# Performance work log

Hardware: AMD Instinct MI355X
Metric: run time of the kernel (lower is better)

Reference implementation:

```python
import jax, jax.numpy as jnp
import numpy as np

HEIGHT, WIDTH = 384, 640


def setup_inputs() -> dict:
    key = jax.random.key(0)
    ks = jax.random.split(key, 6)
    B, N, C_CLS, D = 8, 100, 92, 256
    return {
        "images": jax.random.normal(ks[0], (B, 3, HEIGHT, WIDTH), dtype=jnp.float32),
        "logits": jax.random.normal(ks[1], (B, N, C_CLS), dtype=jnp.float32),
        "pred_boxes": jax.random.uniform(ks[2], (B, N, 4), dtype=jnp.float32),
        "last_hidden_state": jax.random.normal(ks[3], (B, N, D), dtype=jnp.float32),
        "fc_w": jax.random.normal(ks[4], (256, D), dtype=jnp.float32) * 0.05,
        "fc_b": jax.random.normal(ks[5], (256,), dtype=jnp.float32) * 0.05,
    }


def reference(images, logits, pred_boxes, last_hidden_state, fc_w, fc_b):
    B = images.shape[0]
    num_objects = 2

    # probas computed in the original forward (unused in training mode -> DCE'd)
    probas = jax.nn.softmax(logits, axis=-1)[:, :, :-1]

    # cxcywh -> xyxy, scale by [W, H, W, H], truncate to int (torch .int())
    cx, cy, w, h = jnp.split(pred_boxes, 4, axis=-1)  # each [B, N, 1]
    xyxy = jnp.concatenate([cx - 0.5 * w, cy - 0.5 * h, cx + 0.5 * w, cy + 0.5 * h], axis=-1)
    img_dims = jnp.array([WIDTH, HEIGHT, WIDTH, HEIGHT], dtype=jnp.float32)
    bboxes = (xyxy * img_dims).astype(jnp.int32)  # [B, N, 4]

    # bboxes_to_mask (faithful to original, incl. its x/y axis convention):
    # x indexes rows (height), y indexes columns (width)
    x = jnp.arange(HEIGHT, dtype=jnp.float32)[:, None]   # [H, 1]
    y = jnp.arange(WIDTH, dtype=jnp.float32)[None, :]    # [1, W]
    bb = bboxes.astype(jnp.float32)[:, :, :, None, None]  # [B, N, 4, 1, 1]
    masks = (bb[:, :, 0] <= x) & (x <= bb[:, :, 2]) & (bb[:, :, 1] <= y) & (y <= bb[:, :, 3])  # [B, N, H, W]

    # diff images: sum channels, pairwise diff over (pre, post), abs, repeat x2 on batch
    summed = images.sum(axis=1).reshape(B // 2, 2, HEIGHT, WIDTH)
    diff = jnp.abs(summed[:, 1:] - summed[:, :1])          # [B/2, 1, H, W]
    diff = jnp.repeat(diff, 2, axis=0)                     # [B, 1, H, W]

    # masked mean score per box
    scores = jnp.mean(jnp.where(masks, diff, jnp.float32(0.0)), axis=(2, 3))  # [B, N]

    _, indices = jax.lax.top_k(scores, num_objects)        # [B, num_objects]
    h_i = jnp.take_along_axis(last_hidden_state, indices[:, :, None], axis=1)  # [B, O, D]
    h_i = h_i @ fc_w.T + fc_b                              # Linear: x W^T + b
    h_i = h_i.reshape(B // 2, 2, num_objects, -1)          # [b, i=2, O, hidden]
    return h_i[:, 0], h_i[:, 1]
```

## Files before the change

### kernel.cpp

```cpp
#include <hip/hip_runtime.h>

#define H_IMG 384
#define W_IMG 640
#define NPAIR 4
#define NBATCH 8
#define NBOX 100
#define DHID 256
#define ROWTILE 24
#define NTILES (H_IMG / ROWTILE)

__global__ __launch_bounds__(256) void k_diff_rowscan(const float* __restrict__ images,
                                                      float* __restrict__ sat) {
    const int row = blockIdx.x * 4 + (threadIdx.x >> 6);
    const int lane = threadIdx.x & 63;
    const int p = row / H_IMG;
    const int h = row - p * H_IMG;

    const size_t chw = (size_t)H_IMG * W_IMG;
    const float* i0 = images + ((size_t)(2 * p)     * 3 * H_IMG + h) * W_IMG;
    const float* i1 = images + ((size_t)(2 * p + 1) * 3 * H_IMG + h) * W_IMG;
    float* srow = sat + ((size_t)p * H_IMG + h) * W_IMG;

    float carry = 0.0f;
    #pragma unroll
    for (int k = 0; k < W_IMG / 64; ++k) {
        const int w = k * 64 + lane;
        float s0 = (i0[w] + i0[w + chw]) + i0[w + 2 * chw];
        float s1 = (i1[w] + i1[w + chw]) + i1[w + 2 * chw];
        float v = fabsf(s1 - s0);
        #pragma unroll
        for (int off = 1; off < 64; off <<= 1) {
            float u = __shfl_up(v, off, 64);
            if (lane >= off) v += u;
        }
        v += carry;
        srow[w] = v;
        carry = __shfl(v, 63, 64);
    }
}

__global__ __launch_bounds__(64) void k_colscan_local(float* __restrict__ sat,
                                                      float* __restrict__ totals) {
    const int bid = blockIdx.x;
    const int p  = bid / (10 * NTILES);
    const int r1 = bid - p * (10 * NTILES);
    const int t  = r1 / 10;
    const int cg = r1 - t * 10;
    const int c  = cg * 64 + (int)threadIdx.x;

    float* base = sat + ((size_t)p * H_IMG + t * ROWTILE) * W_IMG + c;
    float run = 0.0f;
    #pragma unroll
    for (int i = 0; i < ROWTILE; ++i) {
        run += base[(size_t)i * W_IMG];
        base[(size_t)i * W_IMG] = run;
    }
    totals[((size_t)p * NTILES + t) * W_IMG + c] = run;
}

__global__ __launch_bounds__(256) void k_score_topk_fc(
        const float* __restrict__ sat,
        const float* __restrict__ totals,
        const float* __restrict__ pred_boxes,
        const float* __restrict__ lhs,
        const float* __restrict__ fc_w,
        const float* __restrict__ fc_b,
        float* __restrict__ out) {
    const int b = blockIdx.x;
    const int t = threadIdx.x;
    const int p = b >> 1;

    __shared__ float s_off[NTILES][W_IMG];
    __shared__ float s_score[NBOX];
    __shared__ int   s_idx[2];
    __shared__ float s_h[2][DHID];

    for (int c = t; c < W_IMG; c += 256) {
        float run = 0.0f;
        #pragma unroll
        for (int tt = 0; tt < NTILES; ++tt) {
            s_off[tt][c] = run;
            run += totals[((size_t)p * NTILES + tt) * W_IMG + c];
        }
    }
    __syncthreads();

    const float* S = sat + (size_t)p * H_IMG * W_IMG;

    if (t < NBOX) {
        const float* pb = pred_boxes + ((size_t)b * NBOX + t) * 4;
        const float cx = pb[0], cy = pb[1], bw = pb[2], bh = pb[3];
        const int bb0 = (int)((cx - 0.5f * bw) * 640.0f);
        const int bb1 = (int)((cy - 0.5f * bh) * 384.0f);
        const int bb2 = (int)((cx + 0.5f * bw) * 640.0f);
        const int bb3 = (int)((cy + 0.5f * bh) * 384.0f);
        const int r0 = bb0 > 0 ? bb0 : 0;
        const int r2 = bb2 < H_IMG - 1 ? bb2 : H_IMG - 1;
        const int c0 = bb1 > 0 ? bb1 : 0;
        const int c2 = bb3 < W_IMG - 1 ? bb3 : W_IMG - 1;
        float sc = 0.0f;
        if (r0 <= r2 && c0 <= c2) {
            float sum = S[(size_t)r2 * W_IMG + c2] + s_off[r2 / ROWTILE][c2];
            if (r0 > 0) sum -= S[(size_t)(r0 - 1) * W_IMG + c2] + s_off[(r0 - 1) / ROWTILE][c2];
            if (c0 > 0) sum -= S[(size_t)r2 * W_IMG + (c0 - 1)] + s_off[r2 / ROWTILE][c0 - 1];
            if (r0 > 0 && c0 > 0)
                sum += S[(size_t)(r0 - 1) * W_IMG + (c0 - 1)] + s_off[(r0 - 1) / ROWTILE][c0 - 1];
            sc = sum / (float)(H_IMG * W_IMG);
        }
        s_score[t] = sc;
    }
    __syncthreads();

    if (t == 0) {
        float b0 = -1e30f, b1 = -1e30f;
        int i0 = 0, i1 = 0;
        for (int n = 0; n < NBOX; ++n) {
            const float s = s_score[n];
            if (s > b0)      { b1 = b0; i1 = i0; b0 = s; i0 = n; }
            else if (s > b1) { b1 = s; i1 = n; }
        }
        s_idx[0] = i0;
        s_idx[1] = i1;
    }
    __syncthreads();

    s_h[0][t] = lhs[((size_t)b * NBOX + s_idx[0]) * DHID + t];
    s_h[1][t] = lhs[((size_t)b * NBOX + s_idx[1]) * DHID + t];
    __syncthreads();

    const float* wrow = fc_w + (size_t)t * DHID;
    float acc0 = fc_b[t];
    float acc1 = acc0;
    #pragma unroll 4
    for (int d = 0; d < DHID; ++d) {
        const float wv = wrow[d];
        acc0 = fmaf(s_h[0][d], wv, acc0);
        acc1 = fmaf(s_h[1][d], wv, acc1);
    }

    const size_t base = (size_t)(b & 1) * (NPAIR * 2 * DHID) + (size_t)(b >> 1) * (2 * DHID);
    out[base + t]        = acc0;
    out[base + DHID + t] = acc1;
}

extern "C" void kernel_launch(void* const* d_in, const int* in_sizes, int n_in,
                              void* d_out, int out_size, void* d_ws, size_t ws_size,
                              hipStream_t stream) {
    const float* images     = (const float*)d_in[0];
    const float* pred_boxes = (const float*)d_in[2];
    const float* lhs        = (const float*)d_in[3];
    const float* fc_w       = (const float*)d_in[4];
    const float* fc_b       = (const float*)d_in[5];
    float* out              = (float*)d_out;

    float* sat    = (float*)d_ws;
    float* totals = sat + (size_t)NPAIR * H_IMG * W_IMG;

    hipLaunchKernelGGL(k_diff_rowscan, dim3(NPAIR * H_IMG / 4), dim3(256), 0, stream,
                       images, sat);
    hipLaunchKernelGGL(k_colscan_local, dim3(NPAIR * 10 * NTILES), dim3(64), 0, stream,
                       sat, totals);
    hipLaunchKernelGGL(k_score_topk_fc, dim3(NBATCH), dim3(256), 0, stream,
                       sat, totals, pred_boxes, lhs, fc_w, fc_b, out);
}
```

Baseline: 101.0 us.

## Fuse three kernels into one cooperative kernel with grid syncs

Replaces the three separate launches (diff+row scan, column-tile scan, score/topk/fc) with one cooperative kernel of 256 blocks that loops over the work items and uses grid-wide syncs between the phases. It also vectorises the fc weight loads to float4. The goal is to remove inter-kernel launch gaps. In exchange it adds grid.sync overhead and runs the memory-bound row-scan phase on fewer blocks than before (256 instead of 384), which could reduce achieved bandwidth.

```diff
diff --git a/kernel.cpp b/kernel.cpp
--- a/kernel.cpp
+++ b/kernel.cpp
@@ -1,4 +1,7 @@
 #include <hip/hip_runtime.h>
+#include <hip/hip_cooperative_groups.h>
+
+namespace cg = cooperative_groups;
 
 #define H_IMG 384
 #define W_IMG 640
@@ -8,72 +11,76 @@
 #define DHID 256
 #define ROWTILE 24
 #define NTILES (H_IMG / ROWTILE)
+#define NBLOCKS 256
+#define NWAVES (NBLOCKS * 4)
 
-__global__ __launch_bounds__(256) void k_diff_rowscan(const float* __restrict__ images,
-                                                      float* __restrict__ sat) {
-    const int row = blockIdx.x * 4 + (threadIdx.x >> 6);
-    const int lane = threadIdx.x & 63;
-    const int p = row / H_IMG;
-    const int h = row - p * H_IMG;
-
-    const size_t chw = (size_t)H_IMG * W_IMG;
-    const float* i0 = images + ((size_t)(2 * p)     * 3 * H_IMG + h) * W_IMG;
-    const float* i1 = images + ((size_t)(2 * p + 1) * 3 * H_IMG + h) * W_IMG;
-    float* srow = sat + ((size_t)p * H_IMG + h) * W_IMG;
-
-    float carry = 0.0f;
-    #pragma unroll
-    for (int k = 0; k < W_IMG / 64; ++k) {
-        const int w = k * 64 + lane;
-        float s0 = (i0[w] + i0[w + chw]) + i0[w + 2 * chw];
-        float s1 = (i1[w] + i1[w + chw]) + i1[w + 2 * chw];
-        float v = fabsf(s1 - s0);
-        #pragma unroll
-        for (int off = 1; off < 64; off <<= 1) {
-            float u = __shfl_up(v, off, 64);
-            if (lane >= off) v += u;
-        }
-        v += carry;
-        srow[w] = v;
-        carry = __shfl(v, 63, 64);
-    }
-}
-
-__global__ __launch_bounds__(64) void k_colscan_local(float* __restrict__ sat,
-                                                      float* __restrict__ totals) {
-    const int bid = blockIdx.x;
-    const int p  = bid / (10 * NTILES);
-    const int r1 = bid - p * (10 * NTILES);
-    const int t  = r1 / 10;
-    const int cg = r1 - t * 10;
-    const int c  = cg * 64 + (int)threadIdx.x;
-
-    float* base = sat + ((size_t)p * H_IMG + t * ROWTILE) * W_IMG + c;
-    float run = 0.0f;
-    #pragma unroll
-    for (int i = 0; i < ROWTILE; ++i) {
-        run += base[(size_t)i * W_IMG];
-        base[(size_t)i * W_IMG] = run;
-    }
-    totals[((size_t)p * NTILES + t) * W_IMG + c] = run;
-}
-
-__global__ __launch_bounds__(256) void k_score_topk_fc(
-        const float* __restrict__ sat,
-        const float* __restrict__ totals,
+__global__ __launch_bounds__(256, 1) void k_fused(
+        const float* __restrict__ images,
+        float* __restrict__ sat,
+        float* __restrict__ totals,
         const float* __restrict__ pred_boxes,
         const float* __restrict__ lhs,
         const float* __restrict__ fc_w,
         const float* __restrict__ fc_b,
         float* __restrict__ out) {
-    const int b = blockIdx.x;
+    cg::grid_group grid = cg::this_grid();
     const int t = threadIdx.x;
-    const int p = b >> 1;
+    const int lane = t & 63;
+    const int wid = blockIdx.x * 4 + (t >> 6);
+
+    const size_t chw = (size_t)H_IMG * W_IMG;
+    for (int row = wid; row < NPAIR * H_IMG; row += NWAVES) {
+        const int p = row / H_IMG;
+        const int h = row - p * H_IMG;
+        const float* i0 = images + ((size_t)(2 * p)     * 3 * H_IMG + h) * W_IMG;
+        const float* i1 = images + ((size_t)(2 * p + 1) * 3 * H_IMG + h) * W_IMG;
+        float* srow = sat + ((size_t)p * H_IMG + h) * W_IMG;
+
+        float carry = 0.0f;
+        #pragma unroll
+        for (int k = 0; k < W_IMG / 64; ++k) {
+            const int w = k * 64 + lane;
+            float s0 = (i0[w] + i0[w + chw]) + i0[w + 2 * chw];
+            float s1 = (i1[w] + i1[w + chw]) + i1[w + 2 * chw];
+            float v = fabsf(s1 - s0);
+            #pragma unroll
+            for (int off = 1; off < 64; off <<= 1) {
+                float u = __shfl_up(v, off, 64);
+                if (lane >= off) v += u;
+            }
+            v += carry;
+            srow[w] = v;
+            carry = __shfl(v, 63, 64);
+        }
+    }
+    grid.sync();
+
+    for (int g = wid; g < NPAIR * 10 * NTILES; g += NWAVES) {
+        const int p  = g / (10 * NTILES);
+        const int r1 = g - p * (10 * NTILES);
+        const int tt = r1 / 10;
+        const int cg2 = r1 - tt * 10;
+        const int c  = cg2 * 64 + lane;
+
+        float* base = sat + ((size_t)p * H_IMG + tt * ROWTILE) * W_IMG + c;
+        float run = 0.0f;
+        #pragma unroll
+        for (int i = 0; i < ROWTILE; ++i) {
+            run += base[(size_t)i * W_IMG];
+            base[(size_t)i * W_IMG] = run;
+        }
+        totals[((size_t)p * NTILES + tt) * W_IMG + c] = run;
+    }
+    grid.sync();
 
     __shared__ float s_off[NTILES][W_IMG];
     __shared__ float s_score[NBOX];
     __shared__ int   s_idx[2];
     __shared__ float s_h[2][DHID];
+
+    const int b = blockIdx.x;
+    if (b >= NBATCH) return;
+    const int p = b >> 1;
 
     for (int c = t; c < W_IMG; c += 256) {
         float run = 0.0f;
@@ -128,14 +135,21 @@
     s_h[1][t] = lhs[((size_t)b * NBOX + s_idx[1]) * DHID + t];
     __syncthreads();
 
-    const float* wrow = fc_w + (size_t)t * DHID;
+    const float4* wrow4 = (const float4*)(fc_w + (size_t)t * DHID);
     float acc0 = fc_b[t];
     float acc1 = acc0;
-    #pragma unroll 4
-    for (int d = 0; d < DHID; ++d) {
-        const float wv = wrow[d];
-        acc0 = fmaf(s_h[0][d], wv, acc0);
-        acc1 = fmaf(s_h[1][d], wv, acc1);
+    #pragma unroll 8
+    for (int d4 = 0; d4 < DHID / 4; ++d4) {
+        const float4 wv = wrow4[d4];
+        const int d = d4 * 4;
+        acc0 = fmaf(s_h[0][d + 0], wv.x, acc0);
+        acc0 = fmaf(s_h[0][d + 1], wv.y, acc0);
+        acc0 = fmaf(s_h[0][d + 2], wv.z, acc0);
+        acc0 = fmaf(s_h[0][d + 3], wv.w, acc0);
+        acc1 = fmaf(s_h[1][d + 0], wv.x, acc1);
+        acc1 = fmaf(s_h[1][d + 1], wv.y, acc1);
+        acc1 = fmaf(s_h[1][d + 2], wv.z, acc1);
+        acc1 = fmaf(s_h[1][d + 3], wv.w, acc1);
     }
 
     const size_t base = (size_t)(b & 1) * (NPAIR * 2 * DHID) + (size_t)(b >> 1) * (2 * DHID);
@@ -156,10 +170,8 @@
     float* sat    = (float*)d_ws;
     float* totals = sat + (size_t)NPAIR * H_IMG * W_IMG;
 
-    hipLaunchKernelGGL(k_diff_rowscan, dim3(NPAIR * H_IMG / 4), dim3(256), 0, stream,
-                       images, sat);
-    hipLaunchKernelGGL(k_colscan_local, dim3(NPAIR * 10 * NTILES), dim3(64), 0, stream,
-                       sat, totals);
-    hipLaunchKernelGGL(k_score_topk_fc, dim3(NBATCH), dim3(256), 0, stream,
-                       sat, totals, pred_boxes, lhs, fc_w, fc_b, out);
+    void* args[] = {(void*)&images, (void*)&sat, (void*)&totals, (void*)&pred_boxes,
+                    (void*)&lhs, (void*)&fc_w, (void*)&fc_b, (void*)&out};
+    hipLaunchCooperativeKernel((const void*)k_fused, dim3(NBLOCKS), dim3(256),
+                               args, 0, stream);
 }
```

Result: slower. 184.0 us (+82.3%).
